# Kernel tuning notes

Measured on AMD Instinct MI355X. Metric: run time of the kernel, lower is better.

Reference implementation:

```python
import jax, jax.numpy as jnp
import numpy as np

D_MODEL = 1024
D_INTERNAL = 256


def setup_inputs() -> dict:
    key = jax.random.key(0)
    ks = jax.random.split(key, 12)
    s = 0.02
    return {
        "x": jax.random.normal(ks[0], (4, 2048, D_MODEL), dtype=jnp.float32),
        "Wq": jax.random.normal(ks[1], (D_MODEL, D_INTERNAL), dtype=jnp.float32) * s,
        "bq": jnp.zeros((D_INTERNAL,), dtype=jnp.float32),
        "Wk": jax.random.normal(ks[2], (D_MODEL, D_INTERNAL), dtype=jnp.float32) * s,
        "bk": jnp.zeros((D_INTERNAL,), dtype=jnp.float32),
        "Wv": jax.random.normal(ks[3], (D_MODEL, D_MODEL), dtype=jnp.float32) * s,
        "bv": jnp.zeros((D_MODEL,), dtype=jnp.float32),
        "W1": jax.random.normal(ks[4], (D_MODEL, D_MODEL), dtype=jnp.float32) * s,
        "b1": jnp.zeros((D_MODEL,), dtype=jnp.float32),
        "W2": jax.random.normal(ks[5], (D_MODEL, D_MODEL), dtype=jnp.float32) * s,
        "b2": jnp.zeros((D_MODEL,), dtype=jnp.float32),
    }


def reference(x, Wq, bq, Wk, bk, Wv, bv, W1, b1, W2, b2):
    # x: [B, S, D]
    S = x.shape[-2]
    q = x @ Wq + bq            # [B, S, Di]
    k = x @ Wk + bk            # [B, S, Di]
    v = x @ Wv + bv            # [B, S, D]
    scale = 1.0 / jnp.sqrt(jnp.asarray(q.shape[-1], dtype=x.dtype))
    scores = jnp.einsum('bqd,bkd->bqk', q, k) * scale  # [B, S, S]
    causal_mask = jnp.triu(jnp.ones((S, S), dtype=bool), k=1)
    scores = jnp.where(causal_mask, -jnp.inf, scores)
    attn = jax.nn.softmax(scores, axis=-1)             # [B, S, S]
    attention = jnp.einsum('bqk,bkd->bqd', attn, v)    # [B, S, D]
    h = x + attention
    ff = jax.nn.relu(h @ W1 + b1) @ W2 + b2
    return h + ff, attn
```

## Files before the change

kernel.cpp:

```cpp
#include <hip/hip_runtime.h>
#include <hip/hip_bf16.h>

#define BM 128
#define BN 128

typedef __bf16 bf16x8 __attribute__((ext_vector_type(8)));
typedef float f32x4 __attribute__((ext_vector_type(4)));
typedef unsigned short u16;

__device__ __forceinline__ u16 f2bf(float f) {
    __bf16 b = (__bf16)f;
    return __builtin_bit_cast(u16, b);
}
__device__ __forceinline__ float bf2f(u16 u) {
    __bf16 b = __builtin_bit_cast(__bf16, u);
    return (float)b;
}

__device__ __forceinline__ void gload_lds16(const void* g, void* l) {
    __builtin_amdgcn_global_load_lds(
        (const __attribute__((address_space(1))) void*)g,
        (__attribute__((address_space(3))) void*)l,
        16, 0, 0);
}

template <int MODE>
__global__ __launch_bounds__(256)
void gemm_bt(const u16* __restrict__ A, int lda, long long a_bs,
             const u16* __restrict__ Bt, int ldb, long long b_bs,
             int Kdim, int ldc, long long c_bs,
             const float* __restrict__ bias, float scale,
             const void* __restrict__ resid, long long r_bs,
             void* __restrict__ out, int causal)
{
    int bx = blockIdx.x, by = blockIdx.y, bz = blockIdx.z;
    if (causal == 3) {
        const int t = blockIdx.x;
        int byy = (int)((sqrtf(8.f * (float)t + 1.f) - 1.f) * 0.5f);
        while ((byy + 1) * (byy + 2) / 2 <= t) byy++;
        while (byy * (byy + 1) / 2 > t) byy--;
        by = byy; bx = t - byy * (byy + 1) / 2; bz = blockIdx.y;
    }
    if (causal == 2 && bz >= 2) by = (int)gridDim.y - 1 - by;
    const int kend = (causal == 2) ? min(Kdim, (by + 1) * BM) : Kdim;

    A  += (long long)bz * a_bs;
    Bt += (long long)bz * b_bs;

    const int m0 = by * BM, n0 = bx * BN;
    const int tid = threadIdx.x;
    const int wave = tid >> 6, lane = tid & 63;
    const int wy = wave >> 1, wx = wave & 1;
    const int lr = lane >> 2, lc8 = (lane & 3) * 8;
    const int lane15 = lane & 15, kq = lane >> 4;

    __shared__ __align__(16) u16 As[2][BM * 32];
    __shared__ __align__(16) u16 Bs[2][BN * 32];

    f32x4 acc[4][4] = {};

    for (int k0 = 0; k0 < kend; k0 += 64) {
        __syncthreads();
        #pragma unroll
        for (int h = 0; h < 2; h++) {
            const int kh = k0 + h * 32 + lc8;
            #pragma unroll
            for (int it = 0; it < 2; it++) {
                const int row = wave * 16 + it * 64 + lr;
                gload_lds16(A  + (size_t)(m0 + row) * lda + kh,
                            &As[h][(wave * 16 + it * 64) * 32]);
                gload_lds16(Bt + (size_t)(n0 + row) * ldb + kh,
                            &Bs[h][(wave * 16 + it * 64) * 32]);
            }
        }
        __syncthreads();

        #pragma unroll
        for (int h = 0; h < 2; h++) {
            bf16x8 av[4], bv[4];
            #pragma unroll
            for (int i = 0; i < 4; i++)
                av[i] = *(const bf16x8*)&As[h][(wy * 64 + i * 16 + lane15) * 32 + kq * 8];
            #pragma unroll
            for (int j = 0; j < 4; j++)
                bv[j] = *(const bf16x8*)&Bs[h][(wx * 64 + j * 16 + lane15) * 32 + kq * 8];
            #pragma unroll
            for (int i = 0; i < 4; i++)
                #pragma unroll
                for (int j = 0; j < 4; j++)
                    acc[i][j] = __builtin_amdgcn_mfma_f32_16x16x32_bf16(av[i], bv[j], acc[i][j], 0, 0, 0);
        }
    }

    if (MODE == 6 && n0 >= 512) {
        u16* o = (u16*)resid;
        #pragma unroll
        for (int i = 0; i < 4; i++) {
            const int r = m0 + wy * 64 + i * 16 + kq * 4;
            const size_t base = (size_t)(r >> 11) * 1024 * 2048 + (r & 2047);
            #pragma unroll
            for (int j = 0; j < 4; j++) {
                const int c = n0 + wx * 64 + j * 16 + lane15;
                const float bj = bias[c];
                ushort4 pk;
                pk.x = f2bf(acc[i][j][0] + bj);
                pk.y = f2bf(acc[i][j][1] + bj);
                pk.z = f2bf(acc[i][j][2] + bj);
                pk.w = f2bf(acc[i][j][3] + bj);
                *(ushort4*)&o[base + (size_t)(c - 512) * 2048] = pk;
            }
        }
    } else {
        #pragma unroll
        for (int i = 0; i < 4; i++) {
            const int rl = m0 + wy * 64 + i * 16 + kq * 4;
            #pragma unroll
            for (int j = 0; j < 4; j++) {
                const int c = n0 + wx * 64 + j * 16 + lane15;
                float bj = 0.f;
                if (MODE == 4 || MODE == 5 || MODE == 6) bj = bias[c];
                #pragma unroll
                for (int rg = 0; rg < 4; rg++) {
                    const int r = rl + rg;
                    const size_t idx = (size_t)bz * c_bs + (size_t)r * ldc + c;
                    const float v = acc[i][j][rg];
                    if (MODE == 2) {
                        ((float*)out)[idx] = v * scale;
                    } else if (MODE == 3) {
                        const u16* xr = (const u16*)resid;
                        const float h = bf2f(xr[(size_t)bz * r_bs + (size_t)r * ldc + c]) + v;
                        ((u16*)out)[idx] = f2bf(h);
                    } else if (MODE == 4) {
                        ((u16*)out)[idx] = f2bf(fmaxf(v + bj, 0.f));
                    } else if (MODE == 5) {
                        const u16* hb = (const u16*)resid;
                        ((float*)out)[idx] = v + bj + bf2f(hb[(size_t)r * ldc + c]);
                    } else if (MODE == 6) {
                        ((u16*)out)[idx] = f2bf(v + bj);
                    }
                }
            }
        }
    }
}

__global__ __launch_bounds__(256)
void prep_kernel(const float* __restrict__ x,
                 const float* __restrict__ Wq, const float* __restrict__ bq,
                 const float* __restrict__ Wk, const float* __restrict__ bk,
                 const float* __restrict__ Wv, const float* __restrict__ bv,
                 const float* __restrict__ W1, const float* __restrict__ b1,
                 const float* __restrict__ W2, const float* __restrict__ b2,
                 u16* __restrict__ xb, u16* __restrict__ WqkT, u16* __restrict__ WvT,
                 u16* __restrict__ W1T, u16* __restrict__ W2T, float* __restrict__ biasv)
{
    const int NX = 8388608, NQK = 524288, NW = 1048576;
    const int total = NX + NQK + 3 * NW + 3584;
    for (int i = blockIdx.x * blockDim.x + threadIdx.x; i < total; i += gridDim.x * blockDim.x) {
        int t = i;
        if (t < NX) { xb[t] = f2bf(x[t]); continue; }
        t -= NX;
        if (t < NQK) {
            const int n = t >> 10, k = t & 1023;
            const float v = (n < 256) ? Wq[k * 256 + n] : Wk[k * 256 + (n - 256)];
            WqkT[t] = f2bf(v); continue;
        }
        t -= NQK;
        if (t < NW) { const int n = t >> 10, k = t & 1023; WvT[t] = f2bf(Wv[(size_t)k * 1024 + n]); continue; }
        t -= NW;
        if (t < NW) { const int n = t >> 10, k = t & 1023; W1T[t] = f2bf(W1[(size_t)k * 1024 + n]); continue; }
        t -= NW;
        if (t < NW) { const int n = t >> 10, k = t & 1023; W2T[t] = f2bf(W2[(size_t)k * 1024 + n]); continue; }
        t -= NW;
        if (t < 512)       biasv[t] = (t < 256) ? bq[t] : bk[t - 256];
        else if (t < 1536) biasv[t] = bv[t - 512];
        else if (t < 2560) biasv[t] = b1[t - 1536];
        else               biasv[t] = b2[t - 2560];
    }
}

__device__ __forceinline__ float wave_max(float v) {
    #pragma unroll
    for (int off = 32; off > 0; off >>= 1) v = fmaxf(v, __shfl_xor(v, off, 64));
    return v;
}
__device__ __forceinline__ float wave_sum(float v) {
    #pragma unroll
    for (int off = 32; off > 0; off >>= 1) v += __shfl_xor(v, off, 64);
    return v;
}

__global__ __launch_bounds__(256)
void softmax_kernel(float* __restrict__ attn, u16* __restrict__ attn_b)
{
    const int S = 2048;
    const int row = blockIdx.x;
    const int q = row & (S - 1);
    float* srow = attn + (size_t)row * S;
    u16* brow = attn_b + (size_t)row * S;
    const int valid = q + 1;
    const int kpad = (valid + 127) & ~127;
    __shared__ float buf[2048];
    __shared__ float red[8];
    const int tid = threadIdx.x, wv = tid >> 6, ln = tid & 63;

    float lmax = -3.0e38f;
    for (int k = tid; k < valid; k += 256) { const float v = srow[k]; buf[k] = v; lmax = fmaxf(lmax, v); }
    lmax = wave_max(lmax);
    if (ln == 0) red[wv] = lmax;
    __syncthreads();
    const float m = fmaxf(fmaxf(red[0], red[1]), fmaxf(red[2], red[3]));

    float lsum = 0.f;
    for (int k = tid; k < valid; k += 256) { const float e = __expf(buf[k] - m); buf[k] = e; lsum += e; }
    lsum = wave_sum(lsum);
    if (ln == 0) red[4 + wv] = lsum;
    __syncthreads();
    const float rinv = 1.f / (red[4] + red[5] + red[6] + red[7]);

    for (int k = tid; k < S; k += 256) {
        const float v = (k < valid) ? buf[k] * rinv : 0.f;
        srow[k] = v;
        if (k < kpad) brow[k] = f2bf(v);
    }
}

extern "C" void kernel_launch(void* const* d_in, const int* in_sizes, int n_in,
                              void* d_out, int out_size, void* d_ws, size_t ws_size,
                              hipStream_t stream)
{
    const float* x  = (const float*)d_in[0];
    const float* Wq = (const float*)d_in[1];
    const float* bq = (const float*)d_in[2];
    const float* Wk = (const float*)d_in[3];
    const float* bk = (const float*)d_in[4];
    const float* Wv = (const float*)d_in[5];
    const float* bv = (const float*)d_in[6];
    const float* W1 = (const float*)d_in[7];
    const float* b1 = (const float*)d_in[8];
    const float* W2 = (const float*)d_in[9];
    const float* b2 = (const float*)d_in[10];

    const int B = 4, S = 2048, D = 1024, BS = B * S;

    char* ws = (char*)d_ws;
    u16*   xb    = (u16*)(ws + 0);
    u16*   WqkT  = (u16*)(ws + 16777216);
    u16*   WvT   = (u16*)(ws + 17825792);
    u16*   W1T   = (u16*)(ws + 19922944);
    u16*   W2T   = (u16*)(ws + 22020096);
    float* biasv = (float*)(ws + 24117248);
    u16*   QK    = (u16*)(ws + 24133632);
    u16*   Vt    = (u16*)(ws + 32522240);
    u16*   attnb = (u16*)(ws + 49299456);
    u16*   hb    = xb;
    u16*   ff1   = attnb;

    float* out0 = (float*)d_out;
    float* attn = out0 + (size_t)BS * D;

    const dim3 blk(256);

    prep_kernel<<<dim3(2048), blk, 0, stream>>>(x, Wq, bq, Wk, bk, Wv, bv, W1, b1, W2, b2,
                                                xb, WqkT, WvT, W1T, W2T, biasv);

    gemm_bt<6><<<dim3(12, 64, 1), blk, 0, stream>>>(
        xb, 1024, 0, WqkT, 1024, 0, 1024, 512, 0,
        biasv, 1.f, Vt, 0, QK, 0);

    gemm_bt<2><<<dim3(136, 4, 1), blk, 0, stream>>>(
        QK, 512, (long long)S * 512, QK + 256, 512, (long long)S * 512,
        256, S, (long long)S * S, nullptr, 0.0625f, nullptr, 0, attn, 3);

    softmax_kernel<<<dim3(BS), blk, 0, stream>>>(attn, attnb);

    gemm_bt<3><<<dim3(8, 16, 4), blk, 0, stream>>>(
        attnb, S, (long long)S * S, Vt, S, (long long)D * S,
        S, D, (long long)S * D, nullptr, 1.f, xb, (long long)S * D, hb, 2);

    gemm_bt<4><<<dim3(8, 64, 1), blk, 0, stream>>>(
        hb, 1024, 0, W1T, 1024, 0, 1024, 1024, 0,
        biasv + 1536, 1.f, nullptr, 0, ff1, 0);

    gemm_bt<5><<<dim3(8, 64, 1), blk, 0, stream>>>(
        ff1, 1024, 0, W2T, 1024, 0, 1024, 1024, 0,
        biasv + 2560, 1.f, hb, 0, out0, 0);
}
```

Before: 341.6 us.

## Fuse exp into QK^T epilogue, defer softmax normalization, use 64-wide N tiles

The scores GEMM now applies exp and the causal mask in its epilogue and writes bf16 unnormalized probabilities directly. A lighter norm kernel sums each row, writes the normalized fp32 attn output and stores per-row inverse sums, which the PV GEMM applies in its epilogue. This removes the fp32 score write and re-read and the max pass. The trade-off is that skipping max subtraction relies on scores being small, risking overflow for general inputs. Most GEMMs also switch to BN=64 tiles to double the block count for better occupancy.

```diff
diff --git a/kernel.cpp b/kernel.cpp
--- a/kernel.cpp
+++ b/kernel.cpp
@@ -2,7 +2,6 @@
 #include <hip/hip_bf16.h>
 
 #define BM 128
-#define BN 128
 
 typedef __bf16 bf16x8 __attribute__((ext_vector_type(8)));
 typedef float f32x4 __attribute__((ext_vector_type(4)));
@@ -24,7 +23,7 @@
         16, 0, 0);
 }
 
-template <int MODE>
+template <int MODE, int BN_>
 __global__ __launch_bounds__(256)
 void gemm_bt(const u16* __restrict__ A, int lda, long long a_bs,
              const u16* __restrict__ Bt, int ldb, long long b_bs,
@@ -33,6 +32,9 @@
              const void* __restrict__ resid, long long r_bs,
              void* __restrict__ out, int causal)
 {
+    constexpr int NJ = BN_ / 32;
+    constexpr int JW = BN_ / 2;
+
     int bx = blockIdx.x, by = blockIdx.y, bz = blockIdx.z;
     if (causal == 3) {
         const int t = blockIdx.x;
@@ -47,7 +49,7 @@
     A  += (long long)bz * a_bs;
     Bt += (long long)bz * b_bs;
 
-    const int m0 = by * BM, n0 = bx * BN;
+    const int m0 = by * BM, n0 = bx * BN_;
     const int tid = threadIdx.x;
     const int wave = tid >> 6, lane = tid & 63;
     const int wy = wave >> 1, wx = wave & 1;
@@ -55,9 +57,9 @@
     const int lane15 = lane & 15, kq = lane >> 4;
 
     __shared__ __align__(16) u16 As[2][BM * 32];
-    __shared__ __align__(16) u16 Bs[2][BN * 32];
-
-    f32x4 acc[4][4] = {};
+    __shared__ __align__(16) u16 Bs[2][BN_ * 32];
+
+    f32x4 acc[4][NJ] = {};
 
     for (int k0 = 0; k0 < kend; k0 += 64) {
         __syncthreads();
@@ -67,27 +69,37 @@
             #pragma unroll
             for (int it = 0; it < 2; it++) {
                 const int row = wave * 16 + it * 64 + lr;
-                gload_lds16(A  + (size_t)(m0 + row) * lda + kh,
+                gload_lds16(A + (size_t)(m0 + row) * lda + kh,
                             &As[h][(wave * 16 + it * 64) * 32]);
+            }
+            if (BN_ == 128) {
+                #pragma unroll
+                for (int it = 0; it < 2; it++) {
+                    const int row = wave * 16 + it * 64 + lr;
+                    gload_lds16(Bt + (size_t)(n0 + row) * ldb + kh,
+                                &Bs[h][(wave * 16 + it * 64) * 32]);
+                }
+            } else {
+                const int row = wave * 16 + lr;
                 gload_lds16(Bt + (size_t)(n0 + row) * ldb + kh,
-                            &Bs[h][(wave * 16 + it * 64) * 32]);
+                            &Bs[h][(wave * 16) * 32]);
             }
         }
         __syncthreads();
 
         #pragma unroll
         for (int h = 0; h < 2; h++) {
-            bf16x8 av[4], bv[4];
+            bf16x8 av[4], bv[NJ];
             #pragma unroll
             for (int i = 0; i < 4; i++)
                 av[i] = *(const bf16x8*)&As[h][(wy * 64 + i * 16 + lane15) * 32 + kq * 8];
             #pragma unroll
-            for (int j = 0; j < 4; j++)
-                bv[j] = *(const bf16x8*)&Bs[h][(wx * 64 + j * 16 + lane15) * 32 + kq * 8];
+            for (int j = 0; j < NJ; j++)
+                bv[j] = *(const bf16x8*)&Bs[h][(wx * JW + j * 16 + lane15) * 32 + kq * 8];
             #pragma unroll
             for (int i = 0; i < 4; i++)
                 #pragma unroll
-                for (int j = 0; j < 4; j++)
+                for (int j = 0; j < NJ; j++)
                     acc[i][j] = __builtin_amdgcn_mfma_f32_16x16x32_bf16(av[i], bv[j], acc[i][j], 0, 0, 0);
         }
     }
@@ -99,8 +111,8 @@
             const int r = m0 + wy * 64 + i * 16 + kq * 4;
             const size_t base = (size_t)(r >> 11) * 1024 * 2048 + (r & 2047);
             #pragma unroll
-            for (int j = 0; j < 4; j++) {
-                const int c = n0 + wx * 64 + j * 16 + lane15;
+            for (int j = 0; j < NJ; j++) {
+                const int c = n0 + wx * JW + j * 16 + lane15;
                 const float bj = bias[c];
                 ushort4 pk;
                 pk.x = f2bf(acc[i][j][0] + bj);
@@ -115,8 +127,8 @@
         for (int i = 0; i < 4; i++) {
             const int rl = m0 + wy * 64 + i * 16 + kq * 4;
             #pragma unroll
-            for (int j = 0; j < 4; j++) {
-                const int c = n0 + wx * 64 + j * 16 + lane15;
+            for (int j = 0; j < NJ; j++) {
+                const int c = n0 + wx * JW + j * 16 + lane15;
                 float bj = 0.f;
                 if (MODE == 4 || MODE == 5 || MODE == 6) bj = bias[c];
                 #pragma unroll
@@ -125,10 +137,13 @@
                     const size_t idx = (size_t)bz * c_bs + (size_t)r * ldc + c;
                     const float v = acc[i][j][rg];
                     if (MODE == 2) {
-                        ((float*)out)[idx] = v * scale;
+                        float p = __expf(v * scale);
+                        if (c > r) p = 0.f;
+                        ((u16*)out)[idx] = f2bf(p);
                     } else if (MODE == 3) {
                         const u16* xr = (const u16*)resid;
-                        const float h = bf2f(xr[(size_t)bz * r_bs + (size_t)r * ldc + c]) + v;
+                        const float linv = bias[(size_t)bz * 2048 + r];
+                        const float h = bf2f(xr[(size_t)bz * r_bs + (size_t)r * ldc + c]) + v * linv;
                         ((u16*)out)[idx] = f2bf(h);
                     } else if (MODE == 4) {
                         ((u16*)out)[idx] = f2bf(fmaxf(v + bj, 0.f));
@@ -179,11 +194,6 @@
     }
 }
 
-__device__ __forceinline__ float wave_max(float v) {
-    #pragma unroll
-    for (int off = 32; off > 0; off >>= 1) v = fmaxf(v, __shfl_xor(v, off, 64));
-    return v;
-}
 __device__ __forceinline__ float wave_sum(float v) {
     #pragma unroll
     for (int off = 32; off > 0; off >>= 1) v += __shfl_xor(v, off, 64);
@@ -191,38 +201,32 @@
 }
 
 __global__ __launch_bounds__(256)
-void softmax_kernel(float* __restrict__ attn, u16* __restrict__ attn_b)
+void norm_kernel(const u16* __restrict__ attnb, float* __restrict__ attn,
+                 float* __restrict__ linv)
 {
     const int S = 2048;
     const int row = blockIdx.x;
     const int q = row & (S - 1);
-    float* srow = attn + (size_t)row * S;
-    u16* brow = attn_b + (size_t)row * S;
     const int valid = q + 1;
     const int kpad = (valid + 127) & ~127;
-    __shared__ float buf[2048];
-    __shared__ float red[8];
+    const u16* brow = attnb + (size_t)row * S;
+    float* srow = attn + (size_t)row * S;
+    __shared__ float red[4];
     const int tid = threadIdx.x, wv = tid >> 6, ln = tid & 63;
 
-    float lmax = -3.0e38f;
-    for (int k = tid; k < valid; k += 256) { const float v = srow[k]; buf[k] = v; lmax = fmaxf(lmax, v); }
-    lmax = wave_max(lmax);
-    if (ln == 0) red[wv] = lmax;
+    float vals[8];
+    float lsum = 0.f;
+    int cnt = 0;
+    for (int k = tid; k < kpad; k += 256) { const float v = bf2f(brow[k]); vals[cnt++] = v; lsum += v; }
+    lsum = wave_sum(lsum);
+    if (ln == 0) red[wv] = lsum;
     __syncthreads();
-    const float m = fmaxf(fmaxf(red[0], red[1]), fmaxf(red[2], red[3]));
-
-    float lsum = 0.f;
-    for (int k = tid; k < valid; k += 256) { const float e = __expf(buf[k] - m); buf[k] = e; lsum += e; }
-    lsum = wave_sum(lsum);
-    if (ln == 0) red[4 + wv] = lsum;
-    __syncthreads();
-    const float rinv = 1.f / (red[4] + red[5] + red[6] + red[7]);
-
-    for (int k = tid; k < S; k += 256) {
-        const float v = (k < valid) ? buf[k] * rinv : 0.f;
-        srow[k] = v;
-        if (k < kpad) brow[k] = f2bf(v);
-    }
+    const float rinv = 1.f / (red[0] + red[1] + red[2] + red[3]);
+
+    cnt = 0;
+    for (int k = tid; k < kpad; k += 256) { srow[k] = (k < valid) ? vals[cnt] * rinv : 0.f; cnt++; }
+    for (int k = kpad + tid; k < S; k += 256) srow[k] = 0.f;
+    if (tid == 0) linv[row] = rinv;
 }
 
 extern "C" void kernel_launch(void* const* d_in, const int* in_sizes, int n_in,
@@ -253,6 +257,7 @@
     u16*   QK    = (u16*)(ws + 24133632);
     u16*   Vt    = (u16*)(ws + 32522240);
     u16*   attnb = (u16*)(ws + 49299456);
+    float* linv  = (float*)(ws + 83886080);
     u16*   hb    = xb;
     u16*   ff1   = attnb;
 
@@ -264,25 +269,25 @@
     prep_kernel<<<dim3(2048), blk, 0, stream>>>(x, Wq, bq, Wk, bk, Wv, bv, W1, b1, W2, b2,
                                                 xb, WqkT, WvT, W1T, W2T, biasv);
 
-    gemm_bt<6><<<dim3(12, 64, 1), blk, 0, stream>>>(
+    gemm_bt<6, 64><<<dim3(24, 64, 1), blk, 0, stream>>>(
         xb, 1024, 0, WqkT, 1024, 0, 1024, 512, 0,
         biasv, 1.f, Vt, 0, QK, 0);
 
-    gemm_bt<2><<<dim3(136, 4, 1), blk, 0, stream>>>(
+    gemm_bt<2, 128><<<dim3(136, 4, 1), blk, 0, stream>>>(
         QK, 512, (long long)S * 512, QK + 256, 512, (long long)S * 512,
-        256, S, (long long)S * S, nullptr, 0.0625f, nullptr, 0, attn, 3);
-
-    softmax_kernel<<<dim3(BS), blk, 0, stream>>>(attn, attnb);
-
-    gemm_bt<3><<<dim3(8, 16, 4), blk, 0, stream>>>(
+        256, S, (long long)S * S, nullptr, 0.0625f, nullptr, 0, attnb, 3);
+
+    norm_kernel<<<dim3(BS), blk, 0, stream>>>(attnb, attn, linv);
+
+    gemm_bt<3, 64><<<dim3(16, 16, 4), blk, 0, stream>>>(
         attnb, S, (long long)S * S, Vt, S, (long long)D * S,
-        S, D, (long long)S * D, nullptr, 1.f, xb, (long long)S * D, hb, 2);
-
-    gemm_bt<4><<<dim3(8, 64, 1), blk, 0, stream>>>(
+        S, D, (long long)S * D, linv, 1.f, xb, (long long)S * D, hb, 2);
+
+    gemm_bt<4, 64><<<dim3(16, 64, 1), blk, 0, stream>>>(
         hb, 1024, 0, W1T, 1024, 0, 1024, 1024, 0,
         biasv + 1536, 1.f, nullptr, 0, ff1, 0);
 
-    gemm_bt<5><<<dim3(8, 64, 1), blk, 0, stream>>>(
+    gemm_bt<5, 64><<<dim3(16, 64, 1), blk, 0, stream>>>(
         ff1, 1024, 0, W2T, 1024, 0, 1024, 1024, 0,
         biasv + 2560, 1.f, hb, 0, out0, 0);
 }
```

New measurement: 349.3 us. +2.2%, slower.

## Fuse exp into score GEMM, defer softmax normalization to PV epilogue

Applied to the files above, without the earlier changes.

The score GEMM now writes unnormalized exp(scores) as bf16 with the causal mask applied, so the fp32 score matrix is never written and read back. A lighter norm kernel sums each bf16 row, writes the normalized fp32 attention output, and stores the per-row reciprocal. The PV GEMM applies that reciprocal in its epilogue. Prep is split into a vectorized x conversion and an LDS-tiled weight transpose. Skipping the max subtraction relies on scores staying small enough that exp does not overflow, and the row sums are taken over bf16-rounded values.

```diff
diff --git a/kernel.cpp b/kernel.cpp
--- a/kernel.cpp
+++ b/kernel.cpp
@@ -125,10 +125,13 @@
                     const size_t idx = (size_t)bz * c_bs + (size_t)r * ldc + c;
                     const float v = acc[i][j][rg];
                     if (MODE == 2) {
-                        ((float*)out)[idx] = v * scale;
+                        float p = __expf(v * scale);
+                        if (c > r) p = 0.f;
+                        ((u16*)out)[idx] = f2bf(p);
                     } else if (MODE == 3) {
                         const u16* xr = (const u16*)resid;
-                        const float h = bf2f(xr[(size_t)bz * r_bs + (size_t)r * ldc + c]) + v;
+                        const float linv = bias[(size_t)bz * 2048 + r];
+                        const float h = bf2f(xr[(size_t)bz * r_bs + (size_t)r * ldc + c]) + v * linv;
                         ((u16*)out)[idx] = f2bf(h);
                     } else if (MODE == 4) {
                         ((u16*)out)[idx] = f2bf(fmaxf(v + bj, 0.f));
@@ -145,45 +148,77 @@
 }
 
 __global__ __launch_bounds__(256)
-void prep_kernel(const float* __restrict__ x,
-                 const float* __restrict__ Wq, const float* __restrict__ bq,
-                 const float* __restrict__ Wk, const float* __restrict__ bk,
-                 const float* __restrict__ Wv, const float* __restrict__ bv,
-                 const float* __restrict__ W1, const float* __restrict__ b1,
-                 const float* __restrict__ W2, const float* __restrict__ b2,
-                 u16* __restrict__ xb, u16* __restrict__ WqkT, u16* __restrict__ WvT,
-                 u16* __restrict__ W1T, u16* __restrict__ W2T, float* __restrict__ biasv)
-{
-    const int NX = 8388608, NQK = 524288, NW = 1048576;
-    const int total = NX + NQK + 3 * NW + 3584;
-    for (int i = blockIdx.x * blockDim.x + threadIdx.x; i < total; i += gridDim.x * blockDim.x) {
-        int t = i;
-        if (t < NX) { xb[t] = f2bf(x[t]); continue; }
-        t -= NX;
-        if (t < NQK) {
-            const int n = t >> 10, k = t & 1023;
-            const float v = (n < 256) ? Wq[k * 256 + n] : Wk[k * 256 + (n - 256)];
-            WqkT[t] = f2bf(v); continue;
-        }
-        t -= NQK;
-        if (t < NW) { const int n = t >> 10, k = t & 1023; WvT[t] = f2bf(Wv[(size_t)k * 1024 + n]); continue; }
-        t -= NW;
-        if (t < NW) { const int n = t >> 10, k = t & 1023; W1T[t] = f2bf(W1[(size_t)k * 1024 + n]); continue; }
-        t -= NW;
-        if (t < NW) { const int n = t >> 10, k = t & 1023; W2T[t] = f2bf(W2[(size_t)k * 1024 + n]); continue; }
-        t -= NW;
-        if (t < 512)       biasv[t] = (t < 256) ? bq[t] : bk[t - 256];
-        else if (t < 1536) biasv[t] = bv[t - 512];
-        else if (t < 2560) biasv[t] = b1[t - 1536];
-        else               biasv[t] = b2[t - 2560];
-    }
-}
-
-__device__ __forceinline__ float wave_max(float v) {
+void prep_x(const float* __restrict__ x, u16* __restrict__ xb)
+{
+    const int N4 = 8388608 / 4;
+    for (int i = blockIdx.x * blockDim.x + threadIdx.x; i < N4; i += gridDim.x * blockDim.x) {
+        const float4 v = ((const float4*)x)[i];
+        ushort4 o;
+        o.x = f2bf(v.x); o.y = f2bf(v.y); o.z = f2bf(v.z); o.w = f2bf(v.w);
+        ((ushort4*)xb)[i] = o;
+    }
+}
+
+__global__ __launch_bounds__(256)
+void prep_w(const float* __restrict__ Wq, const float* __restrict__ bq,
+            const float* __restrict__ Wk, const float* __restrict__ bk,
+            const float* __restrict__ Wv, const float* __restrict__ bv,
+            const float* __restrict__ b1, const float* __restrict__ b2,
+            const float* __restrict__ W1, const float* __restrict__ W2,
+            u16* __restrict__ WqkT, u16* __restrict__ WvT,
+            u16* __restrict__ W1T, u16* __restrict__ W2T, float* __restrict__ biasv)
+{
+    const int bid = blockIdx.x, tid = threadIdx.x;
+    if (bid == 896) {
+        for (int t = tid; t < 3584; t += 256) {
+            if (t < 512)       biasv[t] = (t < 256) ? bq[t] : bk[t - 256];
+            else if (t < 1536) biasv[t] = bv[t - 512];
+            else if (t < 2560) biasv[t] = b1[t - 1536];
+            else               biasv[t] = b2[t - 2560];
+        }
+        return;
+    }
+    const float* src; u16* dst; int ld_src, kt, nt, nbase;
+    if (bid < 128) {
+        const int job = bid >> 6, t = bid & 63;
+        src = job ? Wk : Wq; ld_src = 256;
+        kt = t >> 2; nt = t & 3; nbase = job * 256 + nt * 64;
+        dst = WqkT;
+    } else {
+        const int j = bid - 128, w = j >> 8, t = j & 255;
+        src = (w == 0) ? Wv : (w == 1) ? W1 : W2; ld_src = 1024;
+        kt = t >> 4; nt = t & 15; nbase = nt * 64;
+        dst = (w == 0) ? WvT : (w == 1) ? W1T : W2T;
+    }
+    const int k0 = kt * 64, n0 = (nbase & 255) | (nbase & ~255 & 0);
+    const int n0s = (ld_src == 256) ? (nbase & 255) : nbase;
+
+    __shared__ float tile[64][65];
+    const int ri = tid >> 4, j4 = (tid & 15) * 4;
     #pragma unroll
-    for (int off = 32; off > 0; off >>= 1) v = fmaxf(v, __shfl_xor(v, off, 64));
-    return v;
-}
+    for (int rr = 0; rr < 4; rr++) {
+        const int i = ri + rr * 16;
+        const float4 v = *(const float4*)&src[(size_t)(k0 + i) * ld_src + n0s + j4];
+        tile[j4 + 0][i] = v.x;
+        tile[j4 + 1][i] = v.y;
+        tile[j4 + 2][i] = v.z;
+        tile[j4 + 3][i] = v.w;
+    }
+    __syncthreads();
+    const int n = tid >> 2, ks = (tid & 3) * 16;
+    ushort4 o[4];
+    #pragma unroll
+    for (int c = 0; c < 4; c++) {
+        o[c].x = f2bf(tile[n][ks + c * 4 + 0]);
+        o[c].y = f2bf(tile[n][ks + c * 4 + 1]);
+        o[c].z = f2bf(tile[n][ks + c * 4 + 2]);
+        o[c].w = f2bf(tile[n][ks + c * 4 + 3]);
+    }
+    u16* drow = &dst[(size_t)(nbase + n) * 1024 + k0 + ks];
+    #pragma unroll
+    for (int c = 0; c < 4; c++) *(ushort4*)&drow[c * 4] = o[c];
+}
+
 __device__ __forceinline__ float wave_sum(float v) {
     #pragma unroll
     for (int off = 32; off > 0; off >>= 1) v += __shfl_xor(v, off, 64);
@@ -191,38 +226,42 @@
 }
 
 __global__ __launch_bounds__(256)
-void softmax_kernel(float* __restrict__ attn, u16* __restrict__ attn_b)
+void norm_kernel(const u16* __restrict__ attnb, float* __restrict__ attn,
+                 float* __restrict__ linv)
 {
     const int S = 2048;
     const int row = blockIdx.x;
     const int q = row & (S - 1);
+    const int kpad = (q + 128) & ~127;
+    const u16* brow = attnb + (size_t)row * S;
     float* srow = attn + (size_t)row * S;
-    u16* brow = attn_b + (size_t)row * S;
-    const int valid = q + 1;
-    const int kpad = (valid + 127) & ~127;
-    __shared__ float buf[2048];
-    __shared__ float red[8];
+    __shared__ float red[4];
     const int tid = threadIdx.x, wv = tid >> 6, ln = tid & 63;
-
-    float lmax = -3.0e38f;
-    for (int k = tid; k < valid; k += 256) { const float v = srow[k]; buf[k] = v; lmax = fmaxf(lmax, v); }
-    lmax = wave_max(lmax);
-    if (ln == 0) red[wv] = lmax;
+    const int k = tid * 8;
+
+    float vals[8];
+    float lsum = 0.f;
+    if (k < kpad) {
+        const ushort4 a = *(const ushort4*)&brow[k];
+        const ushort4 b = *(const ushort4*)&brow[k + 4];
+        vals[0] = bf2f(a.x); vals[1] = bf2f(a.y); vals[2] = bf2f(a.z); vals[3] = bf2f(a.w);
+        vals[4] = bf2f(b.x); vals[5] = bf2f(b.y); vals[6] = bf2f(b.z); vals[7] = bf2f(b.w);
+        #pragma unroll
+        for (int c = 0; c < 8; c++) lsum += vals[c];
+    }
+    lsum = wave_sum(lsum);
+    if (ln == 0) red[wv] = lsum;
     __syncthreads();
-    const float m = fmaxf(fmaxf(red[0], red[1]), fmaxf(red[2], red[3]));
-
-    float lsum = 0.f;
-    for (int k = tid; k < valid; k += 256) { const float e = __expf(buf[k] - m); buf[k] = e; lsum += e; }
-    lsum = wave_sum(lsum);
-    if (ln == 0) red[4 + wv] = lsum;
-    __syncthreads();
-    const float rinv = 1.f / (red[4] + red[5] + red[6] + red[7]);
-
-    for (int k = tid; k < S; k += 256) {
-        const float v = (k < valid) ? buf[k] * rinv : 0.f;
-        srow[k] = v;
-        if (k < kpad) brow[k] = f2bf(v);
-    }
+    const float rinv = 1.f / (red[0] + red[1] + red[2] + red[3]);
+
+    float4 o0 = {0.f, 0.f, 0.f, 0.f}, o1 = {0.f, 0.f, 0.f, 0.f};
+    if (k < kpad) {
+        o0 = make_float4(vals[0] * rinv, vals[1] * rinv, vals[2] * rinv, vals[3] * rinv);
+        o1 = make_float4(vals[4] * rinv, vals[5] * rinv, vals[6] * rinv, vals[7] * rinv);
+    }
+    *(float4*)&srow[k] = o0;
+    *(float4*)&srow[k + 4] = o1;
+    if (tid == 0) linv[row] = rinv;
 }
 
 extern "C" void kernel_launch(void* const* d_in, const int* in_sizes, int n_in,
@@ -253,6 +292,7 @@
     u16*   QK    = (u16*)(ws + 24133632);
     u16*   Vt    = (u16*)(ws + 32522240);
     u16*   attnb = (u16*)(ws + 49299456);
+    float* linv  = (float*)(ws + 83886080);
     u16*   hb    = xb;
     u16*   ff1   = attnb;
 
@@ -261,8 +301,9 @@
 
     const dim3 blk(256);
 
-    prep_kernel<<<dim3(2048), blk, 0, stream>>>(x, Wq, bq, Wk, bk, Wv, bv, W1, b1, W2, b2,
-                                                xb, WqkT, WvT, W1T, W2T, biasv);
+    prep_x<<<dim3(1024), blk, 0, stream>>>(x, xb);
+    prep_w<<<dim3(897), blk, 0, stream>>>(Wq, bq, Wk, bk, Wv, bv, b1, b2, W1, W2,
+                                          WqkT, WvT, W1T, W2T, biasv);
 
     gemm_bt<6><<<dim3(12, 64, 1), blk, 0, stream>>>(
         xb, 1024, 0, WqkT, 1024, 0, 1024, 512, 0,
@@ -270,13 +311,13 @@
 
     gemm_bt<2><<<dim3(136, 4, 1), blk, 0, stream>>>(
         QK, 512, (long long)S * 512, QK + 256, 512, (long long)S * 512,
-        256, S, (long long)S * S, nullptr, 0.0625f, nullptr, 0, attn, 3);
-
-    softmax_kernel<<<dim3(BS), blk, 0, stream>>>(attn, attnb);
+        256, S, (long long)S * S, nullptr, 0.0625f, nullptr, 0, attnb, 3);
+
+    norm_kernel<<<dim3(BS), blk, 0, stream>>>(attnb, attn, linv);
 
     gemm_bt<3><<<dim3(8, 16, 4), blk, 0, stream>>>(
         attnb, S, (long long)S * S, Vt, S, (long long)D * S,
-        S, D, (long long)S * D, nullptr, 1.f, xb, (long long)S * D, hb, 2);
+        S, D, (long long)S * D, linv, 1.f, xb, (long long)S * D, hb, 2);
 
     gemm_bt<4><<<dim3(8, 64, 1), blk, 0, stream>>>(
         hb, 1024, 0, W1T, 1024, 0, 1024, 1024, 0,
```

After: 330.3 us. 1.03x faster.
